# Optimization experiments

Hardware: AMD Instinct MI355X
Metric: run time of the kernel (lower is better)

## Reference

```python
import jax, jax.numpy as jnp
import numpy as np

B, S, D, H, L, V, C = 2, 1024, 1024, 16, 6, 50257, 2048
HD = D // H  # head dim = 64


def setup_inputs() -> dict:
    key = jax.random.key(0)
    ks = jax.random.split(key, 9)
    n = lambda k, shp: (0.02 * jax.random.normal(k, shp)).astype(jnp.float32)
    return {
        "tokens": jax.random.randint(ks[0], (B, S), 0, V, dtype=jnp.int32),
        "tok_emb": n(ks[1], (V, D)),   # tied with to_logits
        "pos_emb": n(ks[2], (C, D)),
        "ln1_g": jnp.ones((L, D), jnp.float32), "ln1_b": jnp.zeros((L, D), jnp.float32),
        "wq": n(ks[3], (L, D, D)), "wk": n(ks[4], (L, D, D)),
        "wv": n(ks[5], (L, D, D)), "wo": n(ks[6], (L, D, D)),
        "ln2_g": jnp.ones((L, D), jnp.float32), "ln2_b": jnp.zeros((L, D), jnp.float32),
        "w1": n(ks[7], (L, D, 4 * D)), "b1": jnp.zeros((L, 4 * D), jnp.float32),
        "w2": n(ks[8], (L, 4 * D, D)), "b2": jnp.zeros((L, D), jnp.float32),
        "lnf_g": jnp.ones((D,), jnp.float32), "lnf_b": jnp.zeros((D,), jnp.float32),
    }


def _ln(x, g, b):
    m = x.mean(-1, keepdims=True)
    v = x.var(-1, keepdims=True)
    return (x - m) * jax.lax.rsqrt(v + 1e-5) * g + b


def _gpt(tokens, tok_emb, pos_emb, ln1_g, ln1_b, wq, wk, wv, wo,
         ln2_g, ln2_b, w1, b1, w2, b2, lnf_g, lnf_b):
    bs, seq = tokens.shape
    x = tok_emb[tokens] + pos_emb[:seq][None]            # [B,S,D]
    mask = jnp.tril(jnp.ones((seq, seq), dtype=bool))    # causal: True = keep
    scale = 1.0 / np.sqrt(HD)

    def block(x, lp):
        g1, be1, Wq, Wk, Wv, Wo, g2, be2, W1, B1, W2, B2 = lp
        h = _ln(x, g1, be1)
        # project and split heads: [B,S,D] -> [B,H,S,hd]
        q = (h @ Wq).reshape(bs, seq, H, HD).transpose(0, 2, 1, 3)
        k = (h @ Wk).reshape(bs, seq, H, HD).transpose(0, 2, 1, 3)
        v = (h @ Wv).reshape(bs, seq, H, HD).transpose(0, 2, 1, 3)
        scores = jnp.einsum('bhid,bhjd->bhij', q, k) * scale
        scores = jnp.where(mask, scores, -jnp.inf)
        attn = jax.nn.softmax(scores, axis=-1)
        o = jnp.einsum('bhij,bhjd->bhid', attn, v)
        o = o.transpose(0, 2, 1, 3).reshape(bs, seq, D)
        x = x + o @ Wo
        h2 = _ln(x, g2, be2)
        # exact (erf) GELU matches torch nn.GELU default
        x = x + (jax.nn.gelu(h2 @ W1 + B1, approximate=False) @ W2 + B2)
        return x, None

    layer_params = (ln1_g, ln1_b, wq, wk, wv, wo, ln2_g, ln2_b, w1, b1, w2, b2)
    x, _ = jax.lax.scan(block, x, layer_params)
    x = _ln(x, lnf_g, lnf_b)
    return x @ tok_emb.T                                  # tied output head [B,S,V]


def reference(tokens, tok_emb, pos_emb, ln1_g, ln1_b, wq, wk, wv, wo,
              ln2_g, ln2_b, w1, b1, w2, b2, lnf_g, lnf_b):
    return _gpt(tokens, tok_emb, pos_emb, ln1_g, ln1_b, wq, wk, wv, wo,
                ln2_g, ln2_b, w1, b1, w2, b2, lnf_g, lnf_b)
```

## Files before the change

### kernel.cpp

```cpp
#include <hip/hip_runtime.h>
#include <hip/hip_bf16.h>
#include <math.h>

#define BB 2
#define SS 1024
#define DD 1024
#define NHEAD 16
#define HDIM 64
#define NLAYER 6
#define VOCAB 50257
#define DFF 4096
#define BS 2048

typedef __bf16 bf16_t;
typedef __attribute__((ext_vector_type(8))) __bf16 bf16x8;
typedef __attribute__((ext_vector_type(4))) __bf16 bf16x4;
typedef __attribute__((ext_vector_type(4))) float f32x4;

__device__ __forceinline__ f32x4 mfma16(bf16x8 a, bf16x8 b, f32x4 c) {
  return __builtin_amdgcn_mfma_f32_16x16x32_bf16(a, b, c, 0, 0, 0);
}

__device__ __forceinline__ void async16(const void* gp, void* lp) {
  __builtin_amdgcn_global_load_lds(
      (const __attribute__((address_space(1))) unsigned int*)gp,
      (__attribute__((address_space(3))) unsigned int*)lp, 16, 0, 0);
}

__device__ __forceinline__ f32x4 zero4() {
  f32x4 v = {0.f, 0.f, 0.f, 0.f};
  return v;
}

__global__ void k_embed(const int* __restrict__ tokens, const float* __restrict__ tok_emb,
                        const float* __restrict__ pos_emb, float* __restrict__ x) {
  int row = blockIdx.x;
  int s = row & (SS - 1);
  int tk = tokens[row];
  const float4* te = (const float4*)(tok_emb + (size_t)tk * DD);
  const float4* pe = (const float4*)(pos_emb + (size_t)s * DD);
  float4* xo = (float4*)(x + (size_t)row * DD);
  int i = threadIdx.x;
  float4 a = te[i], b = pe[i];
  xo[i] = make_float4(a.x + b.x, a.y + b.y, a.z + b.z, a.w + b.w);
}

__global__ void k_cvt(const float* __restrict__ in, bf16_t* __restrict__ out, long n4) {
  long i = (long)blockIdx.x * blockDim.x + threadIdx.x;
  long stride = (long)gridDim.x * blockDim.x;
  for (; i < n4; i += stride) {
    float4 v = ((const float4*)in)[i];
    bf16x4 o;
    o.x = (bf16_t)v.x; o.y = (bf16_t)v.y; o.z = (bf16_t)v.z; o.w = (bf16_t)v.w;
    ((bf16x4*)out)[i] = o;
  }
}

__global__ void k_transpose_cvt(const float* __restrict__ in, bf16_t* __restrict__ out,
                                int K, int N) {
  __shared__ float tile[32][33];
  int t = threadIdx.x, tx = t & 31, ty = t >> 5;
  int ntile = N >> 5;
  int nt = blockIdx.x % ntile, kt = blockIdx.x / ntile;
  const float* ip = in + (size_t)(kt * 32) * N + nt * 32;
#pragma unroll
  for (int u = 0; u < 4; u++) tile[ty + 8 * u][tx] = ip[(size_t)(ty + 8 * u) * N + tx];
  __syncthreads();
  bf16_t* op = out + (size_t)(nt * 32) * K + kt * 32;
#pragma unroll
  for (int u = 0; u < 4; u++) op[(size_t)(ty + 8 * u) * K + tx] = (bf16_t)tile[tx][ty + 8 * u];
}

__global__ void k_vtrans(const bf16_t* __restrict__ qkv, bf16_t* __restrict__ vt) {
  __shared__ bf16_t tile[32][33];
  int t = threadIdx.x, tx = t & 31, ty = t >> 5;
  int blk = blockIdx.x;
  int dt = blk & 1;  blk >>= 1;
  int st = blk & 31; blk >>= 5;
  int h  = blk & 15; blk >>= 4;
  int b  = blk;
  const bf16_t* ip = qkv + (size_t)(b * SS + st * 32) * (3 * DD) + 2 * DD + h * HDIM + dt * 32;
#pragma unroll
  for (int u = 0; u < 4; u++) tile[ty + 8 * u][tx] = ip[(size_t)(ty + 8 * u) * (3 * DD) + tx];
  __syncthreads();
  bf16_t* op = vt + ((size_t)((b * NHEAD + h) * HDIM + dt * 32)) * SS + st * 32;
#pragma unroll
  for (int u = 0; u < 4; u++) op[(size_t)(ty + 8 * u) * SS + tx] = tile[tx][ty + 8 * u];
}

__global__ void k_ln(const float* __restrict__ x, const float* __restrict__ g,
                     const float* __restrict__ b, bf16_t* __restrict__ out) {
  int row = blockIdx.x, t = threadIdx.x;
  float4 v = ((const float4*)(x + (size_t)row * DD))[t];
  float s = v.x + v.y + v.z + v.w;
  float s2 = v.x * v.x + v.y * v.y + v.z * v.z + v.w * v.w;
#pragma unroll
  for (int m = 32; m >= 1; m >>= 1) { s += __shfl_xor(s, m); s2 += __shfl_xor(s2, m); }
  __shared__ float red[8];
  int w = t >> 6;
  if ((t & 63) == 0) { red[w] = s; red[4 + w] = s2; }
  __syncthreads();
  s = red[0] + red[1] + red[2] + red[3];
  s2 = red[4] + red[5] + red[6] + red[7];
  float mean = s * (1.f / DD);
  float var = s2 * (1.f / DD) - mean * mean;
  float r = rsqrtf(var + 1e-5f);
  float4 gg = ((const float4*)g)[t], bb = ((const float4*)b)[t];
  bf16x4 o;
  o.x = (bf16_t)((v.x - mean) * r * gg.x + bb.x);
  o.y = (bf16_t)((v.y - mean) * r * gg.y + bb.y);
  o.z = (bf16_t)((v.z - mean) * r * gg.z + bb.z);
  o.w = (bf16_t)((v.w - mean) * r * gg.w + bb.w);
  ((bf16x4*)(out + (size_t)row * DD))[t] = o;
}

template <int MODE, bool NB>
__global__ __launch_bounds__(256, 2)
void k_gemm(const bf16_t* __restrict__ A, const bf16_t* __restrict__ Bt,
            int M, int N, int K,
            float* __restrict__ Cf, bf16_t* __restrict__ Cb,
            const float* __restrict__ bias, const float* __restrict__ res) {
  __shared__ bf16_t lA[128 * 32];
  __shared__ bf16_t lB[128 * 32];
  int t = threadIdx.x;
  int m0 = blockIdx.x * 128, n0 = blockIdx.y * 128;
  int lane = t & 63, wvid = t >> 6;
  int wy = wvid >> 1, wx = wvid & 1;
  int lo = lane & 15, hi = lane >> 4;
  f32x4 acc[4][4];
#pragma unroll
  for (int i = 0; i < 4; i++)
#pragma unroll
    for (int j = 0; j < 4; j++) acc[i][j] = zero4();

  int arow = t >> 2;
  int acol = (t & 3) * 8;
  const bf16_t* ap = A + (size_t)(m0 + arow) * K + acol;
  int br0 = n0 + arow, br1 = br0 + 64;
  if (NB) { br0 = min(br0, N - 1); br1 = min(br1, N - 1); }
  const bf16_t* bp0 = Bt + (size_t)br0 * K + acol;
  const bf16_t* bp1 = Bt + (size_t)br1 * K + acol;

  for (int k0 = 0; k0 < K; k0 += 32) {
    async16(ap, &lA[t * 8]);
    async16(ap + (size_t)64 * K, &lA[2048 + t * 8]);
    async16(bp0, &lB[t * 8]);
    async16(bp1, &lB[2048 + t * 8]);
    __syncthreads();
    int kc = hi * 8;
    bf16x8 af[4], bfr[4];
#pragma unroll
    for (int i = 0; i < 4; i++) af[i] = *(const bf16x8*)&lA[(64 * wy + 16 * i + lo) * 32 + kc];
#pragma unroll
    for (int j = 0; j < 4; j++) bfr[j] = *(const bf16x8*)&lB[(64 * wx + 16 * j + lo) * 32 + kc];
#pragma unroll
    for (int i = 0; i < 4; i++)
#pragma unroll
      for (int j = 0; j < 4; j++) acc[i][j] = mfma16(af[i], bfr[j], acc[i][j]);
    __syncthreads();
    ap += 32; bp0 += 32; bp1 += 32;
  }

#pragma unroll
  for (int i = 0; i < 4; i++) {
#pragma unroll
    for (int j = 0; j < 4; j++) {
#pragma unroll
      for (int r = 0; r < 4; r++) {
        int mm = m0 + 64 * wy + 16 * i + 4 * hi + r;
        int nn = n0 + 64 * wx + 16 * j + lo;
        float v = acc[i][j][r];
        size_t idx = (size_t)mm * N + nn;
        if constexpr (MODE == 0) {
          Cb[idx] = (bf16_t)v;
        } else if constexpr (MODE == 1) {
          Cf[idx] = v + res[idx];
        } else if constexpr (MODE == 2) {
          float xx = v + bias[nn];
          Cb[idx] = (bf16_t)(0.5f * xx * (1.f + erff(xx * 0.7071067811865475f)));
        } else if constexpr (MODE == 3) {
          Cf[idx] = v + bias[nn] + res[idx];
        } else {
          if (nn < N) Cf[idx] = v;
        }
      }
    }
  }
}

__global__ __launch_bounds__(256, 1)
void k_attn(const bf16_t* __restrict__ qkv, const bf16_t* __restrict__ vt,
            bf16_t* __restrict__ o) {
  __shared__ bf16_t lQ[128 * 72];
  __shared__ bf16_t lK[64 * 72];
  __shared__ bf16_t lV[64 * 72];
  __shared__ bf16_t lP[128 * 72];
  int t = threadIdx.x;
  int lane = t & 63, w = t >> 6;
  int lo = lane & 15, hi = lane >> 4;
  int blk = blockIdx.x;
  int qt = blk & 7, h = (blk >> 3) & 15, b = blk >> 7;
  int q0 = qt * 128;
  const bf16_t* qbase = qkv + (size_t)(b * SS) * (3 * DD) + h * HDIM;
  const bf16_t* kbase = qbase + DD;
  const bf16_t* vbase = vt + (size_t)((b * NHEAD + h) * HDIM) * SS;

#pragma unroll
  for (int u = 0; u < 4; u++) {
    int c = t + 256 * u;
    int row = c >> 3, col = (c & 7) * 8;
    *(bf16x8*)&lQ[row * 72 + col] = *(const bf16x8*)&qbase[(size_t)(q0 + row) * (3 * DD) + col];
  }

  f32x4 acc_o[2][4];
#pragma unroll
  for (int i2 = 0; i2 < 2; i2++)
#pragma unroll
    for (int j2 = 0; j2 < 4; j2++) acc_o[i2][j2] = zero4();
  float mrow[8], lrow[8];
#pragma unroll
  for (int r = 0; r < 8; r++) { mrow[r] = -1e30f; lrow[r] = 0.f; }

  int nkt = 2 * qt + 2;
  for (int kt = 0; kt < nkt; kt++) {
    int k0 = kt * 64;
    __syncthreads();
#pragma unroll
    for (int u = 0; u < 2; u++) {
      int c = t + 256 * u;
      int row = c >> 3, col = (c & 7) * 8;
      *(bf16x8*)&lK[row * 72 + col] = *(const bf16x8*)&kbase[(size_t)(k0 + row) * (3 * DD) + col];
    }
#pragma unroll
    for (int u = 0; u < 2; u++) {
      int c = t + 256 * u;
      int row = c >> 3, col = (c & 7) * 8;
      *(bf16x8*)&lV[row * 72 + col] = *(const bf16x8*)&vbase[(size_t)row * SS + k0 + col];
    }
    __syncthreads();

    f32x4 sa[2][4];
#pragma unroll
    for (int i2 = 0; i2 < 2; i2++)
#pragma unroll
      for (int j = 0; j < 4; j++) sa[i2][j] = zero4();
#pragma unroll
    for (int kk = 0; kk < 2; kk++) {
      int kc = kk * 32 + hi * 8;
      bf16x8 a0 = *(const bf16x8*)&lQ[(32 * w + lo) * 72 + kc];
      bf16x8 a1 = *(const bf16x8*)&lQ[(32 * w + 16 + lo) * 72 + kc];
#pragma unroll
      for (int j = 0; j < 4; j++) {
        bf16x8 bb = *(const bf16x8*)&lK[(16 * j + lo) * 72 + kc];
        sa[0][j] = mfma16(a0, bb, sa[0][j]);
        sa[1][j] = mfma16(a1, bb, sa[1][j]);
      }
    }

    bool diag = (kt >= 2 * qt);
#pragma unroll
    for (int i2 = 0; i2 < 2; i2++) {
#pragma unroll
      for (int r = 0; r < 4; r++) {
        int ridx = i2 * 4 + r;
        int lrow_i = 32 * w + 16 * i2 + 4 * hi + r;
        int grow = q0 + lrow_i;
        float vals[4];
        float mx = -1e30f;
#pragma unroll
        for (int j = 0; j < 4; j++) {
          float sv = sa[i2][j][r] * 0.125f;
          if (diag && (k0 + 16 * j + lo > grow)) sv = -1e30f;
          vals[j] = sv;
          mx = fmaxf(mx, sv);
        }
#pragma unroll
        for (int mk = 8; mk >= 1; mk >>= 1) mx = fmaxf(mx, __shfl_xor(mx, mk));
        float mo = mrow[ridx];
        float mn = fmaxf(mo, mx);
        float al = __expf(mo - mn);
        float ps = 0.f;
#pragma unroll
        for (int j = 0; j < 4; j++) {
          float pv = __expf(vals[j] - mn);
          ps += pv;
          lP[lrow_i * 72 + 16 * j + lo] = (bf16_t)pv;
        }
#pragma unroll
        for (int mk = 8; mk >= 1; mk >>= 1) ps += __shfl_xor(ps, mk);
        mrow[ridx] = mn;
        lrow[ridx] = lrow[ridx] * al + ps;
#pragma unroll
        for (int j2 = 0; j2 < 4; j2++) acc_o[i2][j2][r] *= al;
      }
    }
    __syncthreads();

#pragma unroll
    for (int kk = 0; kk < 2; kk++) {
      int kc = kk * 32 + hi * 8;
      bf16x8 p0 = *(const bf16x8*)&lP[(32 * w + lo) * 72 + kc];
      bf16x8 p1 = *(const bf16x8*)&lP[(32 * w + 16 + lo) * 72 + kc];
#pragma unroll
      for (int j2 = 0; j2 < 4; j2++) {
        bf16x8 vb = *(const bf16x8*)&lV[(16 * j2 + lo) * 72 + kc];
        acc_o[0][j2] = mfma16(p0, vb, acc_o[0][j2]);
        acc_o[1][j2] = mfma16(p1, vb, acc_o[1][j2]);
      }
    }
  }

  bf16_t* obase = o + (size_t)(b * SS + q0) * DD + h * HDIM;
#pragma unroll
  for (int i2 = 0; i2 < 2; i2++) {
#pragma unroll
    for (int r = 0; r < 4; r++) {
      float inv = 1.f / lrow[i2 * 4 + r];
      int row = 32 * w + 16 * i2 + 4 * hi + r;
#pragma unroll
      for (int j2 = 0; j2 < 4; j2++)
        obase[(size_t)row * DD + 16 * j2 + lo] = (bf16_t)(acc_o[i2][j2][r] * inv);
    }
  }
}

extern "C" void kernel_launch(void* const* d_in, const int* in_sizes, int n_in,
                              void* d_out, int out_size, void* d_ws, size_t ws_size,
                              hipStream_t stream) {
  const int*   tokens  = (const int*)d_in[0];
  const float* tok_emb = (const float*)d_in[1];
  const float* pos_emb = (const float*)d_in[2];
  const float* ln1_g   = (const float*)d_in[3];
  const float* ln1_b   = (const float*)d_in[4];
  const float* wq      = (const float*)d_in[5];
  const float* wk      = (const float*)d_in[6];
  const float* wv      = (const float*)d_in[7];
  const float* wo      = (const float*)d_in[8];
  const float* ln2_g   = (const float*)d_in[9];
  const float* ln2_b   = (const float*)d_in[10];
  const float* w1      = (const float*)d_in[11];
  const float* b1      = (const float*)d_in[12];
  const float* w2      = (const float*)d_in[13];
  const float* b2      = (const float*)d_in[14];
  const float* lnf_g   = (const float*)d_in[15];
  const float* lnf_b   = (const float*)d_in[16];
  float* out = (float*)d_out;

  char* p = (char*)d_ws;
  size_t off = 0;
  auto take = [&](size_t bytes) -> void* {
    void* r = p + off;
    off += (bytes + 255) & ~(size_t)255;
    return r;
  };
  float*  x     = (float*) take((size_t)BS * DD * 4);
  bf16_t* h     = (bf16_t*)take((size_t)BS * DD * 2);
  bf16_t* qkv   = (bf16_t*)take((size_t)BS * 3 * DD * 2);
  bf16_t* vtb   = (bf16_t*)take((size_t)BB * NHEAD * HDIM * SS * 2);
  bf16_t* ob    = (bf16_t*)take((size_t)BS * DD * 2);
  bf16_t* mid   = (bf16_t*)take((size_t)BS * DFF * 2);
  bf16_t* wqkvt = (bf16_t*)take((size_t)3 * DD * DD * 2);
  bf16_t* wot   = (bf16_t*)take((size_t)DD * DD * 2);
  bf16_t* w1t   = (bf16_t*)take((size_t)DD * DFF * 2);
  bf16_t* w2t   = (bf16_t*)take((size_t)DD * DFF * 2);
  bf16_t* te    = (bf16_t*)take((size_t)VOCAB * DD * 2);

  k_cvt<<<8192, 256, 0, stream>>>(tok_emb, te, (long)VOCAB * DD / 4);
  k_embed<<<BS, 256, 0, stream>>>(tokens, tok_emb, pos_emb, x);

  for (int l = 0; l < NLAYER; l++) {
    k_transpose_cvt<<<(DD/32)*(DD/32), 256, 0, stream>>>(wq + (size_t)l*DD*DD, wqkvt, DD, DD);
    k_transpose_cvt<<<(DD/32)*(DD/32), 256, 0, stream>>>(wk + (size_t)l*DD*DD, wqkvt + (size_t)DD*DD, DD, DD);
    k_transpose_cvt<<<(DD/32)*(DD/32), 256, 0, stream>>>(wv + (size_t)l*DD*DD, wqkvt + (size_t)2*DD*DD, DD, DD);
    k_transpose_cvt<<<(DD/32)*(DD/32), 256, 0, stream>>>(wo + (size_t)l*DD*DD, wot, DD, DD);
    k_transpose_cvt<<<(DD/32)*(DFF/32), 256, 0, stream>>>(w1 + (size_t)l*DD*DFF, w1t, DD, DFF);
    k_transpose_cvt<<<(DFF/32)*(DD/32), 256, 0, stream>>>(w2 + (size_t)l*DD*DFF, w2t, DFF, DD);

    k_ln<<<BS, 256, 0, stream>>>(x, ln1_g + (size_t)l*DD, ln1_b + (size_t)l*DD, h);
    k_gemm<0,false><<<dim3(16, 24), 256, 0, stream>>>(h, wqkvt, BS, 3*DD, DD,
                                                      nullptr, qkv, nullptr, nullptr);
    k_vtrans<<<BB*NHEAD*32*2, 256, 0, stream>>>(qkv, vtb);
    k_attn<<<BB*NHEAD*8, 256, 0, stream>>>(qkv, vtb, ob);
    k_gemm<1,false><<<dim3(16, 8), 256, 0, stream>>>(ob, wot, BS, DD, DD,
                                                     x, nullptr, nullptr, x);
    k_ln<<<BS, 256, 0, stream>>>(x, ln2_g + (size_t)l*DD, ln2_b + (size_t)l*DD, h);
    k_gemm<2,false><<<dim3(16, 32), 256, 0, stream>>>(h, w1t, BS, DFF, DD,
                                                      nullptr, mid, b1 + (size_t)l*DFF, nullptr);
    k_gemm<3,false><<<dim3(16, 8), 256, 0, stream>>>(mid, w2t, BS, DD, DFF,
                                                     x, nullptr, b2 + (size_t)l*DD, x);
  }
  k_ln<<<BS, 256, 0, stream>>>(x, lnf_g, lnf_b, h);
  k_gemm<4,true><<<dim3(16, (VOCAB + 127)/128), 256, 0, stream>>>(h, te, BS, VOCAB, DD,
                                                                  out, nullptr, nullptr, nullptr);
}
```

Before: 2.360 ms.

## Add dedicated 256x256 pipelined logits GEMM and merge weight transposes into one launch

Replaces the generic 128-tile GEMM for the vocabulary projection with a 512-thread kernel that uses 256x256 tiles. It double-buffers LDS via async global-to-LDS loads with XOR swizzle, uses explicit waitcnt/barrier interleaving of MFMA with staging, and remaps blocks for L2 locality along M. It also fuses the six per-layer weight transpose-convert launches into one kernel. The aim is to cut the large logits GEMM's memory and latency overhead and the per-layer launch overhead. The cost is hand-tuned synchronisation complexity and clamped out-of-range B rows at the vocab tail.

```diff
diff --git a/kernel.cpp b/kernel.cpp
--- a/kernel.cpp
+++ b/kernel.cpp
@@ -56,12 +56,30 @@
   }
 }
 
-__global__ void k_transpose_cvt(const float* __restrict__ in, bf16_t* __restrict__ out,
-                                int K, int N) {
+__global__ void k_trans_all(const float* __restrict__ wq, const float* __restrict__ wk,
+                            const float* __restrict__ wv, const float* __restrict__ wo,
+                            const float* __restrict__ w1, const float* __restrict__ w2,
+                            bf16_t* __restrict__ wqkvt, bf16_t* __restrict__ wot,
+                            bf16_t* __restrict__ w1t, bf16_t* __restrict__ w2t) {
   __shared__ float tile[32][33];
+  int blk = blockIdx.x;
+  const float* in;
+  bf16_t* out;
+  int K, N, tl;
+  if (blk < 4096) {
+    int m = blk >> 10;
+    tl = blk & 1023;
+    K = DD; N = DD;
+    in = (m == 0) ? wq : (m == 1) ? wk : (m == 2) ? wv : wo;
+    out = (m == 3) ? wot : wqkvt + (size_t)m * DD * DD;
+  } else if (blk < 8192) {
+    tl = blk - 4096; in = w1; out = w1t; K = DD; N = DFF;
+  } else {
+    tl = blk - 8192; in = w2; out = w2t; K = DFF; N = DD;
+  }
+  int ntile = N >> 5;
+  int nt = tl % ntile, kt = tl / ntile;
   int t = threadIdx.x, tx = t & 31, ty = t >> 5;
-  int ntile = N >> 5;
-  int nt = blockIdx.x % ntile, kt = blockIdx.x / ntile;
   const float* ip = in + (size_t)(kt * 32) * N + nt * 32;
 #pragma unroll
   for (int u = 0; u < 4; u++) tile[ty + 8 * u][tx] = ip[(size_t)(ty + 8 * u) * N + tx];
@@ -186,6 +204,170 @@
       }
     }
   }
+}
+
+
+#define NBLK_LOG ((VOCAB + 255) / 256)
+
+#define A_LDSOFF(d, h) ((d) * 16384 + (h) * 8192)
+#define B_LDSOFF(d, h) (32768 + (d) * 16384 + (h) * 8192)
+
+__global__ __launch_bounds__(512, 2)
+void k_gemm_logits(const bf16_t* __restrict__ A, const bf16_t* __restrict__ Bt,
+                   float* __restrict__ C) {
+  constexpr int KD = DD;
+  constexpr int N  = VOCAB;
+  constexpr int NT = KD / 64;
+  __shared__ bf16_t sm[65536];
+
+  int t = threadIdx.x;
+  int lane = t & 63, w = t >> 6;
+  int lo = lane & 15, hi = lane >> 4;
+  int wm = w >> 2, wn = w & 3;
+  int bh = wn >> 1;
+
+  int dlin = blockIdx.y * 8 + blockIdx.x;
+  int tt = (dlin & 7) * NBLK_LOG + (dlin >> 3);
+  int m0 = (tt & 7) * 256;
+  int n0 = (tt >> 3) * 256;
+
+  int srow = (w << 4) + (lane >> 3);
+  int scol = ((lane & 7) ^ (lane >> 3)) << 3;
+  size_t a_off0 = (size_t)(m0 + srow) * KD + scol;
+  size_t a_off1 = a_off0 + (size_t)8 * KD;
+  size_t b_off00, b_off01, b_off10, b_off11;
+  {
+    int r0 = min(n0 + srow,       N - 1);
+    int r1 = min(n0 + srow + 8,   N - 1);
+    int r2 = min(n0 + 128 + srow,     N - 1);
+    int r3 = min(n0 + 128 + srow + 8, N - 1);
+    b_off00 = (size_t)r0 * KD + scol;
+    b_off01 = (size_t)r1 * KD + scol;
+    b_off10 = (size_t)r2 * KD + scol;
+    b_off11 = (size_t)r3 * KD + scol;
+  }
+  int c0 = (w * 2) * 512 + lane * 8;
+  int c1 = c0 + 512;
+
+#define STAGE_A(d, h, tl)                                                             \
+  async16(A + a_off0 + (size_t)(h) * (128 * KD) + (tl) * 64, &sm[A_LDSOFF(d, h) + c0]); \
+  async16(A + a_off1 + (size_t)(h) * (128 * KD) + (tl) * 64, &sm[A_LDSOFF(d, h) + c1]);
+#define STAGE_B(d, h, tl)                                                             \
+  async16(Bt + b_off##h##0 + (tl) * 64, &sm[B_LDSOFF(d, h) + c0]);                    \
+  async16(Bt + b_off##h##1 + (tl) * 64, &sm[B_LDSOFF(d, h) + c1]);
+
+  int su0 = (hi ^ (lo & 7)) << 3;
+  int su1 = ((4 + hi) ^ (lo & 7)) << 3;
+  const bf16_t* aR0 = &sm[A_LDSOFF(0, 0) + wm * 8192 + lo * 64];
+  const bf16_t* aR1 = &sm[A_LDSOFF(1, 0) + wm * 8192 + lo * 64];
+  const bf16_t* bR0 = &sm[B_LDSOFF(0, 0) + bh * 8192 + ((wn & 1) * 64 + lo) * 64];
+  const bf16_t* bR1 = &sm[B_LDSOFF(1, 0) + bh * 8192 + ((wn & 1) * 64 + lo) * 64];
+
+#define LOAD_A4(AR, ROFF)                                            \
+  _Pragma("unroll") for (int i = 0; i < 4; i++) {                    \
+    a[i][0] = *(const bf16x8*)&AR[(ROFF) + i * 1024 + su0];          \
+    a[i][1] = *(const bf16x8*)&AR[(ROFF) + i * 1024 + su1];          \
+  }
+#define LOAD_B2(BR, DST, NOFF)                                       \
+  _Pragma("unroll") for (int j = 0; j < 2; j++) {                    \
+    DST[j][0] = *(const bf16x8*)&BR[(NOFF) + j * 1024 + su0];        \
+    DST[j][1] = *(const bf16x8*)&BR[(NOFF) + j * 1024 + su1];        \
+  }
+#define MFMA_Q(I0, J0, BF)                                                              \
+  __builtin_amdgcn_s_setprio(1);                                                        \
+  _Pragma("unroll") for (int kk = 0; kk < 2; kk++)                                      \
+  _Pragma("unroll") for (int i = 0; i < 4; i++)                                         \
+  _Pragma("unroll") for (int j = 0; j < 2; j++)                                         \
+    acc[(I0) + i][(J0) + j] = mfma16(a[i][kk], BF[j][kk], acc[(I0) + i][(J0) + j]);     \
+  __builtin_amdgcn_s_setprio(0);
+#define BARR __builtin_amdgcn_s_barrier()
+#define LGKM0 do { asm volatile("s_waitcnt lgkmcnt(0)" ::: "memory");                   \
+                   __builtin_amdgcn_sched_barrier(0); } while (0)
+#define VMC4 asm volatile("s_waitcnt vmcnt(4)" ::: "memory")
+
+  bf16x8 a[4][2], b0[2][2], b1[2][2];
+  f32x4 acc[8][4];
+#pragma unroll
+  for (int i = 0; i < 8; i++)
+#pragma unroll
+    for (int j = 0; j < 4; j++) acc[i][j] = zero4();
+
+  STAGE_A(0, 0, 0); STAGE_A(0, 1, 0); STAGE_B(0, 0, 0); STAGE_B(0, 1, 0);
+  STAGE_B(1, 0, 1); STAGE_B(1, 1, 1);
+  VMC4;
+  BARR;
+
+  for (int it = 0; it < NT / 2; ++it) {
+    int T = 2 * it;
+    int tp2 = min(T + 2, NT - 1);
+    int tp3 = min(T + 3, NT - 1);
+
+    LOAD_A4(aR0, 0);
+    LOAD_B2(bR0, b0, 0);
+    STAGE_A(1, 0, T + 1);
+    BARR; LGKM0;
+    MFMA_Q(0, 0, b0);
+    BARR;
+    LOAD_B2(bR0, b1, 2048);
+    STAGE_A(1, 1, T + 1);
+    BARR; LGKM0;
+    MFMA_Q(0, 2, b1);
+    BARR;
+    LOAD_A4(aR0, 4096);
+    STAGE_B(0, 0, tp2);
+    BARR; LGKM0;
+    MFMA_Q(4, 2, b1);
+    BARR;
+    STAGE_B(0, 1, tp2);
+    BARR;
+    MFMA_Q(4, 0, b0);
+    VMC4;
+    BARR;
+
+    LOAD_A4(aR1, 0);
+    LOAD_B2(bR1, b0, 0);
+    STAGE_A(0, 0, tp2);
+    BARR; LGKM0;
+    MFMA_Q(0, 0, b0);
+    BARR;
+    LOAD_B2(bR1, b1, 2048);
+    STAGE_A(0, 1, tp2);
+    BARR; LGKM0;
+    MFMA_Q(0, 2, b1);
+    BARR;
+    LOAD_A4(aR1, 4096);
+    STAGE_B(1, 0, tp3);
+    BARR; LGKM0;
+    MFMA_Q(4, 2, b1);
+    BARR;
+    STAGE_B(1, 1, tp3);
+    BARR;
+    MFMA_Q(4, 0, b0);
+    VMC4;
+    BARR;
+  }
+
+  float* Cw = C + (size_t)(m0 + wm * 128) * N + n0 + wn * 64;
+  int ncol0 = n0 + wn * 64;
+#pragma unroll
+  for (int i = 0; i < 8; i++)
+#pragma unroll
+    for (int j = 0; j < 4; j++)
+#pragma unroll
+      for (int r = 0; r < 4; r++) {
+        int gr = i * 16 + hi * 4 + r;
+        int gc = j * 16 + lo;
+        if (ncol0 + gc < N) Cw[(size_t)gr * N + gc] = acc[i][j][r];
+      }
+
+#undef STAGE_A
+#undef STAGE_B
+#undef LOAD_A4
+#undef LOAD_B2
+#undef MFMA_Q
+#undef BARR
+#undef LGKM0
+#undef VMC4
 }
 
 __global__ __launch_bounds__(256, 1)
@@ -369,12 +551,10 @@
   k_embed<<<BS, 256, 0, stream>>>(tokens, tok_emb, pos_emb, x);
 
   for (int l = 0; l < NLAYER; l++) {
-    k_transpose_cvt<<<(DD/32)*(DD/32), 256, 0, stream>>>(wq + (size_t)l*DD*DD, wqkvt, DD, DD);
-    k_transpose_cvt<<<(DD/32)*(DD/32), 256, 0, stream>>>(wk + (size_t)l*DD*DD, wqkvt + (size_t)DD*DD, DD, DD);
-    k_transpose_cvt<<<(DD/32)*(DD/32), 256, 0, stream>>>(wv + (size_t)l*DD*DD, wqkvt + (size_t)2*DD*DD, DD, DD);
-    k_transpose_cvt<<<(DD/32)*(DD/32), 256, 0, stream>>>(wo + (size_t)l*DD*DD, wot, DD, DD);
-    k_transpose_cvt<<<(DD/32)*(DFF/32), 256, 0, stream>>>(w1 + (size_t)l*DD*DFF, w1t, DD, DFF);
-    k_transpose_cvt<<<(DFF/32)*(DD/32), 256, 0, stream>>>(w2 + (size_t)l*DD*DFF, w2t, DFF, DD);
+    k_trans_all<<<12288, 256, 0, stream>>>(
+        wq + (size_t)l*DD*DD, wk + (size_t)l*DD*DD, wv + (size_t)l*DD*DD,
+        wo + (size_t)l*DD*DD, w1 + (size_t)l*DD*DFF, w2 + (size_t)l*DD*DFF,
+        wqkvt, wot, w1t, w2t);
 
     k_ln<<<BS, 256, 0, stream>>>(x, ln1_g + (size_t)l*DD, ln1_b + (size_t)l*DD, h);
     k_gemm<0,false><<<dim3(16, 24), 256, 0, stream>>>(h, wqkvt, BS, 3*DD, DD,
@@ -390,6 +570,5 @@
                                                      x, nullptr, b2 + (size_t)l*DD, x);
   }
   k_ln<<<BS, 256, 0, stream>>>(x, lnf_g, lnf_b, h);
-  k_gemm<4,true><<<dim3(16, (VOCAB + 127)/128), 256, 0, stream>>>(h, te, BS, VOCAB, DD,
-                                                                  out, nullptr, nullptr, nullptr);
-}
+  k_gemm_logits<<<dim3(8, NBLK_LOG), 512, 0, stream>>>(h, te, out);
+}
```

After: 2.280 ms. -3.4%, faster.
